# Kernel optimization log

Hardware: AMD Instinct MI355X
Metric: run time of the kernel (lower is better)

Reference implementation:

```python
import jax, jax.numpy as jnp
import numpy as np


def to_float8(x, exp_bits=4, mant_bits=3):
    # Faithful port of the torch to_float8: clamp exponent, round mantissa.
    max_exp = 2 ** (exp_bits - 1) - 1
    scale = 2.0 ** mant_bits
    sign = jnp.sign(x)
    xa = jnp.abs(x)
    e = jnp.clip(jnp.floor(jnp.log2(xa + 1e-08)), -max_exp, max_exp)
    p = jnp.exp2(e)
    mant_q = jnp.round((xa / p - 1.0) * scale) / scale
    return sign * (1.0 + mant_q) * p


def setup_inputs() -> dict:
    key = jax.random.key(0)
    k0, k1, k2, k3, k4 = jax.random.split(key, 5)
    Bz, Din, L, N, Dout = 32, 512, 512, 512, 512
    u = jax.random.normal(k0, (Bz, Din, L), jnp.float32)
    # |A| < 1 for a stable length-512 recurrence
    A_diag = jax.random.uniform(k1, (N,), jnp.float32, 0.0, 0.9)
    B = jax.random.normal(k2, (N, Din), jnp.float32) * (1.0 / np.sqrt(Din))
    C = jax.random.normal(k3, (Dout, N), jnp.float32) * (1.0 / np.sqrt(N))
    D = jax.random.normal(k4, (Dout, Din), jnp.float32) * (1.0 / np.sqrt(Din))
    return {"u": u, "A_diag": A_diag, "B": B, "C": C, "D": D}


def reference(u, A_diag, B, C, D):
    int_bits, mant_bits = 4, 3
    q = lambda t: to_float8(t, int_bits, mant_bits)
    A_q = q(A_diag)[None, :]          # [1, N]
    B_q, C_q, D_q = q(B), q(C), q(D)
    Bt = B_q.T                         # [Din, N]
    # row_checksum(B_q.t()): append column of row sums -> constant across steps
    right_cs = jnp.concatenate([Bt, Bt.sum(axis=1, keepdims=True)], axis=1)  # [Din, N+1]
    Bz, Din, L = u.shape
    N = A_diag.shape[0]
    u_t = jnp.transpose(u, (2, 0, 1))  # [L, Bz, Din]

    def step(state, ut):
        # col_checksum(ut): append row of column sums
        left_cs = jnp.concatenate([ut, ut.sum(axis=0, keepdims=True)], axis=0)  # [Bz+1, Din]
        prod_cs = left_cs @ right_cs                 # [Bz+1, N+1] checksum-padded matmul
        right_term = prod_cs[:-1, :-1]               # ut @ B_q.T  (ABFT mask is discarded in forward)
        state_q = q(state * A_q + right_term)        # [Bz, N]
        y = q(state_q @ C_q.T + ut @ D_q.T)          # [Bz, Dout]
        return state_q, y

    state0 = jnp.zeros((Bz, N), u.dtype)
    _, Y = jax.lax.scan(step, state0, u_t)           # [L, Bz, Dout]
    return jnp.transpose(Y, (1, 2, 0))               # [Bz, Dout, L]
```

## Files before the change

### kernel.cpp

```cpp
#include <hip/hip_runtime.h>
#include <hip/hip_bf16.h>


#define DINX 512
#define LSEQ 512
#define NDIM 512

__device__ __forceinline__ float q8(float x) {
    float xa = fabsf(x);
    float w  = __fadd_rn(xa, 1e-8f);
    int e = (int)((__float_as_uint(w) >> 23) & 0xFFu) - 127;
    e = e < -7 ? -7 : (e > 7 ? 7 : e);
    float p    = __int_as_float((unsigned)((e + 127) << 23));
    float invp = __int_as_float((unsigned)((127 - e) << 23));
    float t  = __fmul_rn(__fsub_rn(__fmul_rn(xa, invp), 1.0f), 8.0f);
    float m  = __fmul_rn(rintf(t), 0.125f);
    float r  = __fmul_rn(__fadd_rn(1.0f, m), p);
    return copysignf(r, x);
}

__global__ void quantk(const float* __restrict__ in, float* __restrict__ out, int n) {
    int i = blockIdx.x * blockDim.x + threadIdx.x;
    if (i < n) out[i] = q8(in[i]);
}

__global__ __launch_bounds__(256) void quantT3(const float* __restrict__ B,
                                               const float* __restrict__ C,
                                               const float* __restrict__ D,
                                               float* __restrict__ Bqt,
                                               float* __restrict__ Cqt,
                                               float* __restrict__ Dqt) {
    __shared__ float tl[32][33];
    const float* in = blockIdx.z == 0 ? B : (blockIdx.z == 1 ? C : D);
    float* out      = blockIdx.z == 0 ? Bqt : (blockIdx.z == 1 ? Cqt : Dqt);
    const int r0 = blockIdx.y * 32, c0 = blockIdx.x * 32;
    const int x = threadIdx.x & 31, y = threadIdx.x >> 5;
#pragma unroll
    for (int i = 0; i < 32; i += 8)
        tl[y + i][x] = q8(in[(r0 + y + i) * 512 + c0 + x]);
    __syncthreads();
#pragma unroll
    for (int i = 0; i < 32; i += 8)
        out[(c0 + y + i) * 512 + r0 + x] = tl[x][y + i];
}

__device__ __forceinline__ void gemm_pass(const float* __restrict__ X,
                                          const float* __restrict__ W,
                                          int m0, int n0, int KTOT,
                                          float (&acc)[2][4][2][4],
                                          float (*Xs)[128], float (*Ws)[128],
                                          int tid) {
    const int tx = tid & 15, ty = tid >> 4;
    const int srow = tid >> 4, sseg4 = (tid & 15) * 4;
    const float* xp = X + (size_t)srow * 512 + m0 + sseg4;
    const float* wp = W + (size_t)srow * 512 + n0 + sseg4;
    for (int k0 = 0; k0 < KTOT; k0 += 32) {
        float4 x0 = *(const float4*)xp;
        float4 x1 = *(const float4*)(xp + 64);
        float4 x2 = *(const float4*)(xp + 16 * 512);
        float4 x3 = *(const float4*)(xp + 16 * 512 + 64);
        float4 w0 = *(const float4*)wp;
        float4 w1 = *(const float4*)(wp + 64);
        float4 w2 = *(const float4*)(wp + 16 * 512);
        float4 w3 = *(const float4*)(wp + 16 * 512 + 64);
        xp += 32 * 512; wp += 32 * 512;
        __syncthreads();
        *(float4*)&Xs[srow][sseg4]           = x0;
        *(float4*)&Xs[srow][64 + sseg4]      = x1;
        *(float4*)&Xs[16 + srow][sseg4]      = x2;
        *(float4*)&Xs[16 + srow][64 + sseg4] = x3;
        *(float4*)&Ws[srow][sseg4]           = w0;
        *(float4*)&Ws[srow][64 + sseg4]      = w1;
        *(float4*)&Ws[16 + srow][sseg4]      = w2;
        *(float4*)&Ws[16 + srow][64 + sseg4] = w3;
        __syncthreads();
#pragma unroll
        for (int k = 0; k < 32; ++k) {
            float a[2][4], b[2][4];
            *(float4*)&a[0][0] = *(const float4*)&Xs[k][tx * 4];
            *(float4*)&a[1][0] = *(const float4*)&Xs[k][64 + tx * 4];
            *(float4*)&b[0][0] = *(const float4*)&Ws[k][ty * 4];
            *(float4*)&b[1][0] = *(const float4*)&Ws[k][64 + ty * 4];
#pragma unroll
            for (int p = 0; p < 2; ++p)
#pragma unroll
                for (int i = 0; i < 4; ++i)
#pragma unroll
                    for (int q = 0; q < 2; ++q)
#pragma unroll
                        for (int j = 0; j < 4; ++j)
                            acc[p][i][q][j] = fmaf(a[p][i], b[q][j], acc[p][i][q][j]);
        }
    }
}

__global__ __launch_bounds__(256) void gemm_R(const float* __restrict__ u,
                                              const float* __restrict__ Bqt,
                                              float* __restrict__ R) {
    __shared__ float Xs[32][128];
    __shared__ float Ws[32][128];
    const int b  = blockIdx.z;
    const int t0 = blockIdx.x * 128, n0 = blockIdx.y * 128;
    const int tid = threadIdx.x;
    const int tx = tid & 15, ty = tid >> 4;
    const float* ub = u + (size_t)b * (DINX * LSEQ);
    float acc[2][4][2][4] = {};
    gemm_pass(ub, Bqt, t0, n0, DINX, acc, Xs, Ws, tid);
    float* Rb = R + (size_t)b * (LSEQ * NDIM);
#pragma unroll
    for (int p = 0; p < 2; ++p)
#pragma unroll
        for (int i = 0; i < 4; ++i) {
            float* row = Rb + (size_t)(t0 + p * 64 + tx * 4 + i) * NDIM + n0;
            *(float4*)(row + ty * 4)      = make_float4(acc[p][i][0][0], acc[p][i][0][1],
                                                        acc[p][i][0][2], acc[p][i][0][3]);
            *(float4*)(row + 64 + ty * 4) = make_float4(acc[p][i][1][0], acc[p][i][1][1],
                                                        acc[p][i][1][2], acc[p][i][1][3]);
        }
}

__global__ __launch_bounds__(64) void recur(const float* __restrict__ R,
                                            const float* __restrict__ Aq,
                                            float* __restrict__ S) {
    __shared__ float tile[16][68];
    const int b  = blockIdx.x;
    const int n0 = blockIdx.y * 64;
    const int n  = threadIdx.x;
    const float a = Aq[n0 + n];
    const float* Rb = R + (size_t)b * (LSEQ * NDIM) + n0;
    float* Sb = S + (size_t)b * (NDIM * LSEQ) + (size_t)n0 * LSEQ;
    float s = 0.0f;
    const int c = (n & 3) * 4;
    const int rbase = n >> 2;
    for (int t0 = 0; t0 < LSEQ; t0 += 16) {
#pragma unroll
        for (int tt = 0; tt < 16; ++tt) {
            float r = Rb[(size_t)(t0 + tt) * NDIM + n];
            s = q8(__fadd_rn(__fmul_rn(s, a), r));
            tile[tt][n] = s;
        }
        __syncthreads();
#pragma unroll
        for (int p = 0; p < 4; ++p) {
            int row = p * 16 + rbase;
            float4 v = make_float4(tile[c + 0][row], tile[c + 1][row],
                                   tile[c + 2][row], tile[c + 3][row]);
            *(float4*)(Sb + (size_t)row * LSEQ + t0 + c) = v;
        }
        __syncthreads();
    }
}

__global__ __launch_bounds__(256) void gemm_Y(const float* __restrict__ u,
                                              const float* __restrict__ S,
                                              const float* __restrict__ Cqt,
                                              const float* __restrict__ Dqt,
                                              float* __restrict__ Y) {
    __shared__ float Xs[32][128];
    __shared__ float Ws[32][128];
    const int b  = blockIdx.z;
    const int t0 = blockIdx.x * 128, o0 = blockIdx.y * 128;
    const int tid = threadIdx.x;
    const int tx = tid & 15, ty = tid >> 4;
    const float* Sb = S + (size_t)b * (NDIM * LSEQ);
    const float* ub = u + (size_t)b * (DINX * LSEQ);
    float acc[2][4][2][4] = {};
    float c1[2][4][2][4];
    gemm_pass(Sb, Cqt, t0, o0, NDIM, acc, Xs, Ws, tid);
#pragma unroll
    for (int p = 0; p < 2; ++p)
#pragma unroll
        for (int i = 0; i < 4; ++i)
#pragma unroll
            for (int q = 0; q < 2; ++q)
#pragma unroll
                for (int j = 0; j < 4; ++j) {
                    c1[p][i][q][j] = acc[p][i][q][j];
                    acc[p][i][q][j] = 0.0f;
                }
    gemm_pass(ub, Dqt, t0, o0, DINX, acc, Xs, Ws, tid);

    float* Yb = Y + (size_t)b * (NDIM * LSEQ);
#pragma unroll
    for (int q = 0; q < 2; ++q)
#pragma unroll
        for (int j = 0; j < 4; ++j) {
            float y0[4], y1[4];
#pragma unroll
            for (int i = 0; i < 4; ++i) {
                y0[i] = q8(__fadd_rn(c1[0][i][q][j], acc[0][i][q][j]));
                y1[i] = q8(__fadd_rn(c1[1][i][q][j], acc[1][i][q][j]));
            }
            float* row = Yb + (size_t)(o0 + q * 64 + ty * 4 + j) * LSEQ + t0;
            *(float4*)(row + tx * 4)      = make_float4(y0[0], y0[1], y0[2], y0[3]);
            *(float4*)(row + 64 + tx * 4) = make_float4(y1[0], y1[1], y1[2], y1[3]);
        }
}

extern "C" void kernel_launch(void* const* d_in, const int* in_sizes, int n_in,
                              void* d_out, int out_size, void* d_ws, size_t ws_size,
                              hipStream_t stream) {
    const float* u = (const float*)d_in[0];
    const float* A = (const float*)d_in[1];
    const float* B = (const float*)d_in[2];
    const float* C = (const float*)d_in[3];
    const float* D = (const float*)d_in[4];

    float* ws  = (float*)d_ws;
    float* Aq  = ws;
    float* Bqt = Aq + 512;
    float* Cqt = Bqt + 262144;
    float* Dqt = Cqt + 262144;
    float* R   = Dqt + 262144;
    float* S   = R + 8388608;
    float* Y   = (float*)d_out;

    quantk<<<2, 256, 0, stream>>>(A, Aq, 512);
    quantT3<<<dim3(16, 16, 3), 256, 0, stream>>>(B, C, D, Bqt, Cqt, Dqt);

    gemm_R<<<dim3(4, 4, 32), 256, 0, stream>>>(u, Bqt, R);
    recur<<<dim3(32, 8), 64, 0, stream>>>(R, Aq, S);
    gemm_Y<<<dim3(4, 4, 32), 256, 0, stream>>>(u, S, Cqt, Dqt, Y);
}
```

Baseline: 388.8 us.

## Move u·Dᵀ GEMM before recurrence and fold A quantization into weight kernel

The u·D_q^T product is now computed together with u·B_q^T in a single batched GEMM launch of twice the grid, writing a partial Y into the output buffer. The final GEMM computes only S·C_q^T and adds the stored partial before quantizing. This halves the work after the serial recurrence and gives the first GEMM a larger grid, at the cost of an extra read and write of Y through global memory. The quantization of A is merged into the transpose-quantize kernel, removing one launch, and the first GEMM also gets a launch_bounds occupancy hint.

```diff
diff --git a/kernel.cpp b/kernel.cpp
--- a/kernel.cpp
+++ b/kernel.cpp
@@ -19,18 +19,19 @@
     return copysignf(r, x);
 }
 
-__global__ void quantk(const float* __restrict__ in, float* __restrict__ out, int n) {
-    int i = blockIdx.x * blockDim.x + threadIdx.x;
-    if (i < n) out[i] = q8(in[i]);
-}
-
-__global__ __launch_bounds__(256) void quantT3(const float* __restrict__ B,
-                                               const float* __restrict__ C,
-                                               const float* __restrict__ D,
-                                               float* __restrict__ Bqt,
-                                               float* __restrict__ Cqt,
-                                               float* __restrict__ Dqt) {
+__global__ __launch_bounds__(256) void quantT3A(const float* __restrict__ B,
+                                                const float* __restrict__ C,
+                                                const float* __restrict__ D,
+                                                const float* __restrict__ A,
+                                                float* __restrict__ Bqt,
+                                                float* __restrict__ Cqt,
+                                                float* __restrict__ Dqt,
+                                                float* __restrict__ Aq) {
     __shared__ float tl[32][33];
+    if (blockIdx.z == 0 && blockIdx.x == 0 && blockIdx.y == 0) {
+        Aq[threadIdx.x]       = q8(A[threadIdx.x]);
+        Aq[256 + threadIdx.x] = q8(A[256 + threadIdx.x]);
+    }
     const float* in = blockIdx.z == 0 ? B : (blockIdx.z == 1 ? C : D);
     float* out      = blockIdx.z == 0 ? Bqt : (blockIdx.z == 1 ? Cqt : Dqt);
     const int r0 = blockIdx.y * 32, c0 = blockIdx.x * 32;
@@ -94,29 +95,48 @@
     }
 }
 
-__global__ __launch_bounds__(256) void gemm_R(const float* __restrict__ u,
-                                              const float* __restrict__ Bqt,
-                                              float* __restrict__ R) {
+__global__ __launch_bounds__(256, 4) void gemm_RD(const float* __restrict__ u,
+                                                  const float* __restrict__ Bqt,
+                                                  const float* __restrict__ Dqt,
+                                                  float* __restrict__ R,
+                                                  float* __restrict__ Pd) {
     __shared__ float Xs[32][128];
     __shared__ float Ws[32][128];
-    const int b  = blockIdx.z;
+    const int zz = blockIdx.z;
+    const int b  = zz & 31;
+    const bool isR = zz < 32;
     const int t0 = blockIdx.x * 128, n0 = blockIdx.y * 128;
     const int tid = threadIdx.x;
     const int tx = tid & 15, ty = tid >> 4;
     const float* ub = u + (size_t)b * (DINX * LSEQ);
+    const float* Wm = isR ? Bqt : Dqt;
     float acc[2][4][2][4] = {};
-    gemm_pass(ub, Bqt, t0, n0, DINX, acc, Xs, Ws, tid);
-    float* Rb = R + (size_t)b * (LSEQ * NDIM);
-#pragma unroll
-    for (int p = 0; p < 2; ++p)
-#pragma unroll
-        for (int i = 0; i < 4; ++i) {
-            float* row = Rb + (size_t)(t0 + p * 64 + tx * 4 + i) * NDIM + n0;
-            *(float4*)(row + ty * 4)      = make_float4(acc[p][i][0][0], acc[p][i][0][1],
-                                                        acc[p][i][0][2], acc[p][i][0][3]);
-            *(float4*)(row + 64 + ty * 4) = make_float4(acc[p][i][1][0], acc[p][i][1][1],
-                                                        acc[p][i][1][2], acc[p][i][1][3]);
-        }
+    gemm_pass(ub, Wm, t0, n0, DINX, acc, Xs, Ws, tid);
+    if (isR) {
+        float* Rb = R + (size_t)b * (LSEQ * NDIM);
+#pragma unroll
+        for (int p = 0; p < 2; ++p)
+#pragma unroll
+            for (int i = 0; i < 4; ++i) {
+                float* row = Rb + (size_t)(t0 + p * 64 + tx * 4 + i) * NDIM + n0;
+                *(float4*)(row + ty * 4)      = make_float4(acc[p][i][0][0], acc[p][i][0][1],
+                                                            acc[p][i][0][2], acc[p][i][0][3]);
+                *(float4*)(row + 64 + ty * 4) = make_float4(acc[p][i][1][0], acc[p][i][1][1],
+                                                            acc[p][i][1][2], acc[p][i][1][3]);
+            }
+    } else {
+        float* Yb = Pd + (size_t)b * (NDIM * LSEQ);
+#pragma unroll
+        for (int q = 0; q < 2; ++q)
+#pragma unroll
+            for (int j = 0; j < 4; ++j) {
+                float* row = Yb + (size_t)(n0 + q * 64 + ty * 4 + j) * LSEQ + t0;
+                *(float4*)(row + tx * 4)      = make_float4(acc[0][0][q][j], acc[0][1][q][j],
+                                                            acc[0][2][q][j], acc[0][3][q][j]);
+                *(float4*)(row + 64 + tx * 4) = make_float4(acc[1][0][q][j], acc[1][1][q][j],
+                                                            acc[1][2][q][j], acc[1][3][q][j]);
+            }
+    }
 }
 
 __global__ __launch_bounds__(64) void recur(const float* __restrict__ R,
@@ -151,11 +171,9 @@
     }
 }
 
-__global__ __launch_bounds__(256) void gemm_Y(const float* __restrict__ u,
-                                              const float* __restrict__ S,
-                                              const float* __restrict__ Cqt,
-                                              const float* __restrict__ Dqt,
-                                              float* __restrict__ Y) {
+__global__ __launch_bounds__(256) void gemm_YC(const float* __restrict__ S,
+                                               const float* __restrict__ Cqt,
+                                               float* __restrict__ Y) {
     __shared__ float Xs[32][128];
     __shared__ float Ws[32][128];
     const int b  = blockIdx.z;
@@ -163,37 +181,27 @@
     const int tid = threadIdx.x;
     const int tx = tid & 15, ty = tid >> 4;
     const float* Sb = S + (size_t)b * (NDIM * LSEQ);
-    const float* ub = u + (size_t)b * (DINX * LSEQ);
     float acc[2][4][2][4] = {};
-    float c1[2][4][2][4];
     gemm_pass(Sb, Cqt, t0, o0, NDIM, acc, Xs, Ws, tid);
-#pragma unroll
-    for (int p = 0; p < 2; ++p)
-#pragma unroll
-        for (int i = 0; i < 4; ++i)
-#pragma unroll
-            for (int q = 0; q < 2; ++q)
-#pragma unroll
-                for (int j = 0; j < 4; ++j) {
-                    c1[p][i][q][j] = acc[p][i][q][j];
-                    acc[p][i][q][j] = 0.0f;
-                }
-    gemm_pass(ub, Dqt, t0, o0, DINX, acc, Xs, Ws, tid);
 
     float* Yb = Y + (size_t)b * (NDIM * LSEQ);
 #pragma unroll
     for (int q = 0; q < 2; ++q)
 #pragma unroll
         for (int j = 0; j < 4; ++j) {
-            float y0[4], y1[4];
-#pragma unroll
-            for (int i = 0; i < 4; ++i) {
-                y0[i] = q8(__fadd_rn(c1[0][i][q][j], acc[0][i][q][j]));
-                y1[i] = q8(__fadd_rn(c1[1][i][q][j], acc[1][i][q][j]));
-            }
             float* row = Yb + (size_t)(o0 + q * 64 + ty * 4 + j) * LSEQ + t0;
-            *(float4*)(row + tx * 4)      = make_float4(y0[0], y0[1], y0[2], y0[3]);
-            *(float4*)(row + 64 + tx * 4) = make_float4(y1[0], y1[1], y1[2], y1[3]);
+            float4 v0 = *(const float4*)(row + tx * 4);
+            float4 v1 = *(const float4*)(row + 64 + tx * 4);
+            *(float4*)(row + tx * 4) =
+                make_float4(q8(__fadd_rn(acc[0][0][q][j], v0.x)),
+                            q8(__fadd_rn(acc[0][1][q][j], v0.y)),
+                            q8(__fadd_rn(acc[0][2][q][j], v0.z)),
+                            q8(__fadd_rn(acc[0][3][q][j], v0.w)));
+            *(float4*)(row + 64 + tx * 4) =
+                make_float4(q8(__fadd_rn(acc[1][0][q][j], v1.x)),
+                            q8(__fadd_rn(acc[1][1][q][j], v1.y)),
+                            q8(__fadd_rn(acc[1][2][q][j], v1.z)),
+                            q8(__fadd_rn(acc[1][3][q][j], v1.w)));
         }
 }
 
@@ -215,10 +223,8 @@
     float* S   = R + 8388608;
     float* Y   = (float*)d_out;
 
-    quantk<<<2, 256, 0, stream>>>(A, Aq, 512);
-    quantT3<<<dim3(16, 16, 3), 256, 0, stream>>>(B, C, D, Bqt, Cqt, Dqt);
-
-    gemm_R<<<dim3(4, 4, 32), 256, 0, stream>>>(u, Bqt, R);
+    quantT3A<<<dim3(16, 16, 3), 256, 0, stream>>>(B, C, D, A, Bqt, Cqt, Dqt, Aq);
+    gemm_RD<<<dim3(4, 4, 64), 256, 0, stream>>>(u, Bqt, Dqt, R, Y);
     recur<<<dim3(32, 8), 64, 0, stream>>>(R, Aq, S);
-    gemm_Y<<<dim3(4, 4, 32), 256, 0, stream>>>(u, S, Cqt, Dqt, Y);
-}
+    gemm_YC<<<dim3(4, 4, 32), 256, 0, stream>>>(S, Cqt, Y);
+}
```

Result: no change. 393.3 us (+1.2%).
